# Optimization experiments

Hardware: AMD Instinct MI355X
Metric: run time of the kernel (lower is better)

Reference implementation:

```python
import jax, jax.numpy as jnp
import numpy as np

C_V, C_F, C_D = 10, 64, 16
COSTS = jnp.array([10.0, 5.0, 2.0], dtype=jnp.float32)  # bandwidth cost per granularity
PENALTY = 0.0  # no_transmission_utility_penalty


def setup_inputs() -> dict:
    key = jax.random.key(0)
    k1, k2 = jax.random.split(key)
    B, H, W = 4, 192, 192
    collab = jax.random.normal(k1, (B, C_V + C_F + C_D, H, W), dtype=jnp.float32)
    utility = jax.random.normal(k2, (B, H, W, 3), dtype=jnp.float32)
    return {"collab_bev_data_list": collab, "utility_map_list": utility,
            "bandwidth_budget": 200000}


def _selection_mechanism(utility, budget_per_sample):
    # utility: [B, H, W, G]; returns [B, H, W] float selected granularity (-1 = none)
    B, H, W, G = utility.shape
    best_u = jnp.max(utility, axis=3)                      # [B,H,W]
    best_g = jnp.argmax(utility, axis=3)                   # [B,H,W]
    N = B * H * W
    flat_u = best_u.reshape(N)
    flat_g = best_g.reshape(N)
    b_idx = jnp.repeat(jnp.arange(B, dtype=jnp.int32), H * W)
    valid = flat_u > PENALTY
    cost = COSTS[flat_g]                                   # [N]
    # sort candidates by utility, descending (stable, matching list.sort)
    order = jnp.argsort(-flat_u)
    v_s = valid[order]
    c_s = cost[order]
    b_s = b_idx[order]

    # greedy budget-constrained selection per sample (sequential knapsack)
    def step(usage, item):
        v, c, b = item
        ok = v & (usage[b] + c <= budget_per_sample)
        usage = usage.at[b].add(jnp.where(ok, c, jnp.float32(0)))
        return usage, ok

    _, sel_sorted = jax.lax.scan(step, jnp.zeros((B,), jnp.float32), (v_s, c_s, b_s))
    selected = jnp.zeros((N,), bool).at[order].set(sel_sorted)
    idx = jnp.where(selected, flat_g.astype(jnp.float32), jnp.float32(-1.0))
    return idx.reshape(B, H, W)


def _build_sparse_bev(sel_idx, vox, feat, det):
    m0 = (sel_idx == 0.0)[:, None, :, :]
    m1 = (sel_idx == 1.0)[:, None, :, :]
    m2 = (sel_idx == 2.0)[:, None, :, :]
    return jnp.concatenate([vox * m0, feat * m1, det * m2], axis=1)


def reference(collab_bev_data_list, utility_map_list, bandwidth_budget):
    cav_num = collab_bev_data_list.shape[0]
    budget_per_sample = jnp.float32(bandwidth_budget / cav_num)
    sel_idx = _selection_mechanism(utility_map_list, budget_per_sample)
    vox = collab_bev_data_list[:, :C_V]
    feat = collab_bev_data_list[:, C_V:C_V + C_F]
    det = collab_bev_data_list[:, C_V + C_F:C_V + C_F + C_D]
    sparse = _build_sparse_bev(sel_idx, vox, feat, det)
    return sparse, sel_idx
```

## Files before the change

### kernel.cpp

```cpp
#include <hip/hip_runtime.h>
#include <stdint.h>
#include <math.h>

#define B_    4
#define H_    192
#define W_    192
#define HW    (H_*W_)
#define NPIX  (B_*HW)
#define C_V   10
#define C_F   64
#define C_D   16
#define C_ALL (C_V+C_F+C_D)
#define HBINS 32768
#define CAP   2048

#define OFF_HIST 0u
#define OFF_KEY  (4u*HBINS*4u)
#define OFF_G    (OFF_KEY + (uint32_t)NPIX*4u)
#define OFF_SELX (OFF_G + (uint32_t)NPIX)
#define OFF_HL   (OFF_SELX + (uint32_t)NPIX)

__device__ __forceinline__ uint32_t costOf(uint32_t g) {
    return g == 0u ? 10u : (g == 1u ? 5u : 2u);
}

__device__ __forceinline__ uint32_t budgetInt(const int* bptr) {
    double bps = (double)bptr[0] / (double)B_;
    float f = (float)bps;
    return (uint32_t)floorf(f);
}

#define CE(x, y) { uint64_t _mn = (x) < (y) ? (x) : (y); \
                   uint64_t _mx = (x) < (y) ? (y) : (x); (x) = _mx; (y) = _mn; }

__global__ void k_zero(uint4* __restrict__ hist4) {
    int i = blockIdx.x * blockDim.x + threadIdx.x;
    hist4[i] = make_uint4(0u, 0u, 0u, 0u);
}

__global__ void k_prep(const float* __restrict__ util, uint4* __restrict__ key4,
                       uint32_t* __restrict__ g4, uint32_t* __restrict__ selx4,
                       uint32_t* __restrict__ hist) {
    int t = blockIdx.x * blockDim.x + threadIdx.x;
    if (t >= NPIX / 4) return;
    const float4* u4 = (const float4*)util + (size_t)t * 3;
    float4 a = u4[0], b4 = u4[1], c4 = u4[2];
    float u[4][3] = { {a.x, a.y, a.z}, {a.w, b4.x, b4.y},
                      {b4.z, b4.w, c4.x}, {c4.y, c4.z, c4.w} };
    uint32_t kk[4]; uint32_t gpack = 0;
    #pragma unroll
    for (int p = 0; p < 4; ++p) {
        float best = u[p][0]; uint32_t g = 0;
        if (u[p][1] > best) { best = u[p][1]; g = 1; }
        if (u[p][2] > best) { best = u[p][2]; g = 2; }
        kk[p] = (best > 0.0f) ? (__float_as_uint(best) | 0x80000000u) : 0u;
        gpack |= g << (8 * p);
    }
    key4[t] = make_uint4(kk[0], kk[1], kk[2], kk[3]);
    g4[t] = gpack;
    selx4[t] = 0u;
    int b = (t * 4) / HW;
    #pragma unroll
    for (int p = 0; p < 4; ++p)
        if (kk[p])
            atomicAdd(&hist[(size_t)b * HBINS + ((kk[p] >> 16) & 32767u)],
                      costOf((gpack >> (8 * p)) & 3u));
}

__global__ __launch_bounds__(1024) void k_select(const uint32_t* __restrict__ key,
                                                 const uint8_t* __restrict__ g,
                                                 const uint32_t* __restrict__ hist,
                                                 const int* __restrict__ budget_ptr,
                                                 uint8_t* __restrict__ selx,
                                                 uint32_t* __restrict__ hl_out) {
    int b = blockIdx.x;
    int t = threadIdx.x;
    int lane = t & 63, wv = t >> 6;
    uint32_t budget = budgetInt(budget_ptr);

    __shared__ uint64_t e[CAP];
    __shared__ uint64_t s[CAP];
    __shared__ uint32_t wsum[16];
    __shared__ uint64_t red5[16];
    __shared__ uint64_t red2[16][4];
    __shared__ uint64_t cand[5];
    __shared__ uint32_t f_b2, f_usage, sh_n, sh_r;

    if (t == 0) { f_b2 = 0xFFFFFFFFu; f_usage = 0u; sh_n = 0u; }
    __syncthreads();

    const uint32_t* hb = hist + (size_t)b * HBINS;
    int hi = 32767 - 32 * t;
    uint32_t cs = 0;
    #pragma unroll 4
    for (int j = 0; j < 32; ++j) cs += hb[hi - j];
    uint32_t v = cs;
    #pragma unroll
    for (int off = 1; off < 64; off <<= 1) {
        uint32_t o = __shfl_up(v, off);
        if (lane >= off) v += o;
    }
    if (lane == 63) wsum[wv] = v;
    __syncthreads();
    if (t < 16) {
        uint32_t w = wsum[t];
        #pragma unroll
        for (int off = 1; off < 16; off <<= 1) {
            uint32_t o = __shfl_up(w, off);
            if (t >= off) w += o;
        }
        wsum[t] = w;
    }
    __syncthreads();
    uint32_t incl = v + (wv ? wsum[wv - 1] : 0u);
    uint32_t excl = incl - cs;
    if (excl <= budget && incl > budget) {
        uint32_t cum = excl;
        for (int j = 0; j < 32; ++j) {
            uint32_t hv = hb[hi - j];
            if (cum + hv > budget) { f_b2 = (uint32_t)(hi - j); f_usage = cum; break; }
            cum += hv;
        }
    }
    __syncthreads();
    uint32_t b2 = f_b2;
    if (t == 0) {
        uint32_t hl;
        if (b2 == 0xFFFFFFFFu)           hl = 1u;
        else {
            uint32_t bs = b2 + 32768u;
            hl = (bs >= 65535u) ? 0xFFFFFFFFu : ((bs + 1u) << 16);
        }
        hl_out[b] = hl;
    }
    if (b2 == 0xFFFFFFFFu) return;

    const uint32_t* kb = key + (size_t)b * HW;
    const uint8_t*  gb = g   + (size_t)b * HW;
    uint64_t m5 = 0;
    uint64_t a0 = 0, a1 = 0, a2 = 0, a3 = 0;
    for (int i = t; i < HW; i += 1024) {
        uint32_t k = kb[i];
        if (!k) continue;
        uint32_t bin = (k >> 16) & 32767u;
        if (bin == b2) {
            uint32_t idx = atomicAdd(&sh_n, 1u);
            if (idx < CAP)
                e[idx] = ((uint64_t)(~k) << 32) | ((uint64_t)i << 2) | (uint64_t)gb[i];
        } else if (bin < b2) {
            uint32_t gg = gb[i];
            if (gg == 0u) continue;
            uint64_t m = ((uint64_t)k << 18) | ((uint64_t)(65535u - (uint32_t)i) << 2)
                       | (uint64_t)gg;
            if (gg == 1u) { if (m > m5) m5 = m; }
            else {
                if (m > a3) {
                    if      (m > a0) { a3 = a2; a2 = a1; a1 = a0; a0 = m; }
                    else if (m > a1) { a3 = a2; a2 = a1; a1 = m; }
                    else if (m > a2) { a3 = a2; a2 = m; }
                    else             { a3 = m; }
                }
            }
        }
    }
    #pragma unroll
    for (int off = 32; off; off >>= 1) {
        uint64_t o5 = __shfl_down(m5, off);
        if (o5 > m5) m5 = o5;
        uint64_t b0 = __shfl_down(a0, off), b1 = __shfl_down(a1, off),
                 b2_ = __shfl_down(a2, off), b3 = __shfl_down(a3, off);
        CE(a0, b3); CE(a1, b2_); CE(a2, b1); CE(a3, b0);
        CE(a0, a2); CE(a1, a3); CE(a0, a1); CE(a2, a3);
    }
    if (lane == 0) {
        red5[wv] = m5;
        red2[wv][0] = a0; red2[wv][1] = a1; red2[wv][2] = a2; red2[wv][3] = a3;
    }
    __syncthreads();
    int n = (int)(sh_n < (uint32_t)CAP ? sh_n : (uint32_t)CAP);

    for (int i = t; i < n; i += 1024) {
        uint64_t ei = e[i];
        int rk = 0;
        for (int j = 0; j < n; ++j) rk += (e[j] < ei);
        s[rk] = ei;
    }
    __syncthreads();

    if (t == 0) {
        uint32_t usage = f_usage;
        uint8_t* sx = selx + (size_t)b * HW;
        for (int i = 0; i < n; ++i) {
            uint64_t ei = s[i];
            uint32_t c = costOf((uint32_t)(ei & 3u));
            if (usage + c <= budget) { usage += c; sx[(ei >> 2) & 0xFFFFu] = 1; }
        }
        uint64_t g5 = 0, t0 = 0, t1 = 0, t2 = 0, t3 = 0;
        for (int wq = 0; wq < 16; ++wq) {
            if (red5[wq] > g5) g5 = red5[wq];
            #pragma unroll
            for (int q = 0; q < 4; ++q) {
                uint64_t m = red2[wq][q];
                if (m > t3) {
                    if      (m > t0) { t3 = t2; t2 = t1; t1 = t0; t0 = m; }
                    else if (m > t1) { t3 = t2; t2 = t1; t1 = m; }
                    else if (m > t2) { t3 = t2; t2 = m; }
                    else             { t3 = m; }
                }
            }
        }
        cand[0] = g5; cand[1] = t0; cand[2] = t1; cand[3] = t2; cand[4] = t3;
        for (int i = 1; i < 5; ++i) {
            uint64_t x = cand[i]; int j = i;
            while (j > 0 && cand[j - 1] < x) { cand[j] = cand[j - 1]; --j; }
            cand[j] = x;
        }
        uint32_t r = budget - usage;
        for (int i = 0; i < 5; ++i) {
            uint64_t m = cand[i];
            if (!m) break;
            uint32_t c = costOf((uint32_t)(m & 3u));
            if (c <= r) {
                r -= c;
                uint32_t pix = 65535u - (uint32_t)((m >> 2) & 0xFFFFu);
                sx[pix] = 1;
            }
        }
        sh_r = r; (void)sh_r;
    }
}

__global__ void k_sparse(const float* __restrict__ collab, const uint4* __restrict__ key4,
                         const uint32_t* __restrict__ g4, const uint32_t* __restrict__ selx4,
                         const uint32_t* __restrict__ hl_arr,
                         float* __restrict__ out, float* __restrict__ selOut) {
    int tid = blockIdx.x * blockDim.x + threadIdx.x;
    int c = blockIdx.y, b = blockIdx.z;
    int cls = (c < C_V) ? 0 : ((c < C_V + C_F) ? 1 : 2);
    uint32_t hl = hl_arr[b];
    size_t p4 = (size_t)b * (HW / 4) + (size_t)tid;
    uint4 kk = key4[p4];
    uint32_t gg = g4[p4];
    uint32_t sx = selx4[p4];
    int sc[4];
    uint32_t kv[4] = { kk.x, kk.y, kk.z, kk.w };
    #pragma unroll
    for (int p = 0; p < 4; ++p) {
        bool se = (kv[p] >= hl) || (((sx >> (8 * p)) & 0xFFu) != 0u);
        sc[p] = se ? (int)((gg >> (8 * p)) & 3u) : -1;
    }
    size_t co = ((size_t)(b * C_ALL + c)) * HW + (size_t)tid * 4;
    float4 v = *(const float4*)(collab + co);
    float4 o;
    o.x = (sc[0] == cls) ? v.x : 0.0f;
    o.y = (sc[1] == cls) ? v.y : 0.0f;
    o.z = (sc[2] == cls) ? v.z : 0.0f;
    o.w = (sc[3] == cls) ? v.w : 0.0f;
    *(float4*)(out + co) = o;
    if (c == 0) {
        float4 sf = make_float4((float)sc[0], (float)sc[1], (float)sc[2], (float)sc[3]);
        ((float4*)selOut)[p4] = sf;
    }
}

extern "C" void kernel_launch(void* const* d_in, const int* in_sizes, int n_in,
                              void* d_out, int out_size, void* d_ws, size_t ws_size,
                              hipStream_t stream) {
    (void)in_sizes; (void)n_in; (void)out_size; (void)ws_size;
    const float* collab = (const float*)d_in[0];
    const float* util   = (const float*)d_in[1];
    const int*   budget = (const int*)d_in[2];

    uint8_t*  ws   = (uint8_t*)d_ws;
    uint32_t* hist = (uint32_t*)(ws + OFF_HIST);
    uint32_t* key  = (uint32_t*)(ws + OFF_KEY);
    uint8_t*  g    = ws + OFF_G;
    uint8_t*  selx = ws + OFF_SELX;
    uint32_t* hl   = (uint32_t*)(ws + OFF_HL);

    float* outSparse = (float*)d_out;
    float* outSel    = outSparse + (size_t)B_ * C_ALL * HW;

    k_zero  <<<(4 * HBINS / 4) / 256, 256, 0, stream>>>((uint4*)hist);
    k_prep  <<<(NPIX / 4 + 255) / 256, 256, 0, stream>>>(util, (uint4*)key,
                                                         (uint32_t*)g, (uint32_t*)selx, hist);
    k_select<<<B_, 1024, 0, stream>>>(key, g, hist, budget, selx, hl);
    dim3 grid3(HW / 4 / 256, C_ALL, B_);
    k_sparse<<<grid3, 256, 0, stream>>>(collab, (const uint4*)key, (const uint32_t*)g,
                                        (const uint32_t*)selx, hl, outSparse, outSel);
}
```

Before: 107.5 us.

## Split per-sample selection kernel into coarse cut, parallel gather and final pass

Replaces the single 4-block selection kernel with three stages. A two-level histogram (a 256-bin coarse histogram plus the fine one) locates the budget cutoff bin with one wave per sample. A gather kernel spread over 36 slices per sample collects boundary-bin items and top candidates through global atomics and lists. A small final kernel ranks the boundary items and applies the greedy fill. This is meant to remove the serial scan over the whole image done by only four blocks, at the cost of two extra launches, extra coarse-histogram atomics and global-memory round trips.

```diff
diff --git a/kernel.cpp b/kernel.cpp
--- a/kernel.cpp
+++ b/kernel.cpp
@@ -12,13 +12,21 @@
 #define C_D   16
 #define C_ALL (C_V+C_F+C_D)
 #define HBINS 32768
+#define CBINS 256
 #define CAP   2048
-
-#define OFF_HIST 0u
-#define OFF_KEY  (4u*HBINS*4u)
-#define OFF_G    (OFF_KEY + (uint32_t)NPIX*4u)
-#define OFF_SELX (OFF_G + (uint32_t)NPIX)
-#define OFF_HL   (OFF_SELX + (uint32_t)NPIX)
+#define NSLICE 36
+#define NCAND (NSLICE*5)
+
+#define OFF_HIST   0u
+#define OFF_COARSE (4u*HBINS*4u)
+#define ZERO_U4    ((OFF_COARSE + 4u*CBINS*4u)/16u)
+#define OFF_KEY    (OFF_COARSE + 4u*CBINS*4u)
+#define OFF_G      (OFF_KEY + (uint32_t)NPIX*4u)
+#define OFF_SELX   (OFF_G + (uint32_t)NPIX)
+#define OFF_RES    (OFF_SELX + (uint32_t)NPIX)
+#define OFF_GCNT   (OFF_RES + 48u)
+#define OFF_GLIST  (OFF_GCNT + 16u)
+#define OFF_CAND   (OFF_GLIST + 4u*CAP*8u)
 
 __device__ __forceinline__ uint32_t costOf(uint32_t g) {
     return g == 0u ? 10u : (g == 1u ? 5u : 2u);
@@ -33,14 +41,14 @@
 #define CE(x, y) { uint64_t _mn = (x) < (y) ? (x) : (y); \
                    uint64_t _mx = (x) < (y) ? (y) : (x); (x) = _mx; (y) = _mn; }
 
-__global__ void k_zero(uint4* __restrict__ hist4) {
-    int i = blockIdx.x * blockDim.x + threadIdx.x;
-    hist4[i] = make_uint4(0u, 0u, 0u, 0u);
+__global__ void k_zero(uint4* __restrict__ w4) {
+    uint32_t i = blockIdx.x * blockDim.x + threadIdx.x;
+    if (i < ZERO_U4) w4[i] = make_uint4(0u, 0u, 0u, 0u);
 }
 
 __global__ void k_prep(const float* __restrict__ util, uint4* __restrict__ key4,
                        uint32_t* __restrict__ g4, uint32_t* __restrict__ selx4,
-                       uint32_t* __restrict__ hist) {
+                       uint32_t* __restrict__ hist, uint32_t* __restrict__ coarse) {
     int t = blockIdx.x * blockDim.x + threadIdx.x;
     if (t >= NPIX / 4) return;
     const float4* u4 = (const float4*)util + (size_t)t * 3;
@@ -62,104 +70,114 @@
     int b = (t * 4) / HW;
     #pragma unroll
     for (int p = 0; p < 4; ++p)
-        if (kk[p])
-            atomicAdd(&hist[(size_t)b * HBINS + ((kk[p] >> 16) & 32767u)],
-                      costOf((gpack >> (8 * p)) & 3u));
-}
-
-__global__ __launch_bounds__(1024) void k_select(const uint32_t* __restrict__ key,
-                                                 const uint8_t* __restrict__ g,
-                                                 const uint32_t* __restrict__ hist,
-                                                 const int* __restrict__ budget_ptr,
-                                                 uint8_t* __restrict__ selx,
-                                                 uint32_t* __restrict__ hl_out) {
-    int b = blockIdx.x;
+        if (kk[p]) {
+            uint32_t c = costOf((gpack >> (8 * p)) & 3u);
+            atomicAdd(&hist[(size_t)b * HBINS + ((kk[p] >> 16) & 32767u)], c);
+            atomicAdd(&coarse[(size_t)b * CBINS + ((kk[p] >> 23) & 0xFFu)], c);
+        }
+}
+
+__global__ __launch_bounds__(256) void k_cut(const uint32_t* __restrict__ coarse,
+                                             const uint32_t* __restrict__ hist,
+                                             const int* __restrict__ budget_ptr,
+                                             uint32_t* __restrict__ res,
+                                             uint32_t* __restrict__ gcnt) {
     int t = threadIdx.x;
-    int lane = t & 63, wv = t >> 6;
+    int b = t >> 6, lane = t & 63;
     uint32_t budget = budgetInt(budget_ptr);
 
-    __shared__ uint64_t e[CAP];
-    __shared__ uint64_t s[CAP];
-    __shared__ uint32_t wsum[16];
-    __shared__ uint64_t red5[16];
-    __shared__ uint64_t red2[16][4];
-    __shared__ uint64_t cand[5];
-    __shared__ uint32_t f_b2, f_usage, sh_n, sh_r;
-
-    if (t == 0) { f_b2 = 0xFFFFFFFFu; f_usage = 0u; sh_n = 0u; }
-    __syncthreads();
-
-    const uint32_t* hb = hist + (size_t)b * HBINS;
-    int hi = 32767 - 32 * t;
-    uint32_t cs = 0;
-    #pragma unroll 4
-    for (int j = 0; j < 32; ++j) cs += hb[hi - j];
+    const uint32_t* cb_ = coarse + (size_t)b * CBINS;
+    int hi = 255 - 4 * lane;
+    uint32_t c0 = cb_[hi], c1 = cb_[hi - 1], c2 = cb_[hi - 2], c3 = cb_[hi - 3];
+    uint32_t cs = c0 + c1 + c2 + c3;
     uint32_t v = cs;
     #pragma unroll
     for (int off = 1; off < 64; off <<= 1) {
         uint32_t o = __shfl_up(v, off);
         if (lane >= off) v += o;
     }
-    if (lane == 63) wsum[wv] = v;
-    __syncthreads();
-    if (t < 16) {
-        uint32_t w = wsum[t];
-        #pragma unroll
-        for (int off = 1; off < 16; off <<= 1) {
-            uint32_t o = __shfl_up(w, off);
-            if (t >= off) w += o;
-        }
-        wsum[t] = w;
-    }
-    __syncthreads();
-    uint32_t incl = v + (wv ? wsum[wv - 1] : 0u);
-    uint32_t excl = incl - cs;
-    if (excl <= budget && incl > budget) {
+    uint32_t excl = v - cs;
+    bool found = (excl <= budget) && (v > budget);
+    uint32_t cbin = 0, cusage = 0;
+    if (found) {
         uint32_t cum = excl;
-        for (int j = 0; j < 32; ++j) {
-            uint32_t hv = hb[hi - j];
-            if (cum + hv > budget) { f_b2 = (uint32_t)(hi - j); f_usage = cum; break; }
-            cum += hv;
-        }
-    }
-    __syncthreads();
-    uint32_t b2 = f_b2;
-    if (t == 0) {
-        uint32_t hl;
-        if (b2 == 0xFFFFFFFFu)           hl = 1u;
-        else {
-            uint32_t bs = b2 + 32768u;
-            hl = (bs >= 65535u) ? 0xFFFFFFFFu : ((bs + 1u) << 16);
-        }
-        hl_out[b] = hl;
-    }
+        if      (cum + c0 > budget) { cbin = (uint32_t)hi;     cusage = cum; }
+        else if ((cum += c0) + c1 > budget) { cbin = (uint32_t)(hi - 1); cusage = cum; }
+        else if ((cum += c1) + c2 > budget) { cbin = (uint32_t)(hi - 2); cusage = cum; }
+        else                        { cbin = (uint32_t)(hi - 3); cusage = cum + c2; }
+    }
+    unsigned long long msk = __ballot(found);
+    if (msk == 0ull) {
+        if (lane == 0) { res[b] = 0xFFFFFFFFu; res[4 + b] = 0u; res[8 + b] = 1u;
+                         gcnt[b] = 0u; }
+        return;
+    }
+    int src = __ffsll((long long)msk) - 1;
+    cbin   = __shfl(cbin, src);
+    cusage = __shfl(cusage, src);
+
+    const uint32_t* hb = hist + (size_t)b * HBINS + (size_t)cbin * 128;
+    int fhi = 127 - 2 * lane;
+    uint32_t f0 = hb[fhi], f1 = hb[fhi - 1];
+    uint32_t fs = f0 + f1;
+    v = fs;
+    #pragma unroll
+    for (int off = 1; off < 64; off <<= 1) {
+        uint32_t o = __shfl_up(v, off);
+        if (lane >= off) v += o;
+    }
+    excl = cusage + v - fs;
+    found = (excl <= budget) && (excl + fs > budget);
+    uint32_t b2 = 0, fusage = 0;
+    if (found) {
+        if (excl + f0 > budget) { b2 = cbin * 128u + (uint32_t)fhi;       fusage = excl; }
+        else                    { b2 = cbin * 128u + (uint32_t)(fhi - 1); fusage = excl + f0; }
+    }
+    msk = __ballot(found);
+    src = __ffsll((long long)msk) - 1;
+    b2     = __shfl(b2, src);
+    fusage = __shfl(fusage, src);
+    if (lane == 0) {
+        res[b]     = b2;
+        res[4 + b] = fusage;
+        uint32_t bs = b2 + 32768u;
+        res[8 + b] = (bs >= 65535u) ? 0xFFFFFFFFu : ((bs + 1u) << 16);
+        gcnt[b] = 0u;
+    }
+}
+
+__global__ __launch_bounds__(1024) void k_gather(const uint32_t* __restrict__ key,
+                                                 const uint8_t* __restrict__ g,
+                                                 const uint32_t* __restrict__ res,
+                                                 uint32_t* __restrict__ gcnt,
+                                                 uint64_t* __restrict__ glist,
+                                                 uint64_t* __restrict__ cand) {
+    int b = blockIdx.y;
+    uint32_t b2 = res[b];
     if (b2 == 0xFFFFFFFFu) return;
-
-    const uint32_t* kb = key + (size_t)b * HW;
-    const uint8_t*  gb = g   + (size_t)b * HW;
-    uint64_t m5 = 0;
-    uint64_t a0 = 0, a1 = 0, a2 = 0, a3 = 0;
-    for (int i = t; i < HW; i += 1024) {
-        uint32_t k = kb[i];
-        if (!k) continue;
+    int t = threadIdx.x;
+    int lane = t & 63, wv = t >> 6;
+    uint32_t pix = blockIdx.x * 1024u + (uint32_t)t;
+
+    __shared__ uint64_t red5[16];
+    __shared__ uint64_t red2[16][4];
+
+    uint32_t k = key[(size_t)b * HW + pix];
+    uint64_t m5 = 0, a0 = 0, a1 = 0, a2 = 0, a3 = 0;
+    if (k) {
         uint32_t bin = (k >> 16) & 32767u;
         if (bin == b2) {
-            uint32_t idx = atomicAdd(&sh_n, 1u);
+            uint32_t gg = g[(size_t)b * HW + pix];
+            uint32_t idx = atomicAdd(&gcnt[b], 1u);
             if (idx < CAP)
-                e[idx] = ((uint64_t)(~k) << 32) | ((uint64_t)i << 2) | (uint64_t)gb[i];
+                glist[(size_t)b * CAP + idx] =
+                    ((uint64_t)(~k) << 32) | ((uint64_t)pix << 2) | (uint64_t)gg;
         } else if (bin < b2) {
-            uint32_t gg = gb[i];
-            if (gg == 0u) continue;
-            uint64_t m = ((uint64_t)k << 18) | ((uint64_t)(65535u - (uint32_t)i) << 2)
-                       | (uint64_t)gg;
-            if (gg == 1u) { if (m > m5) m5 = m; }
-            else {
-                if (m > a3) {
-                    if      (m > a0) { a3 = a2; a2 = a1; a1 = a0; a0 = m; }
-                    else if (m > a1) { a3 = a2; a2 = a1; a1 = m; }
-                    else if (m > a2) { a3 = a2; a2 = m; }
-                    else             { a3 = m; }
-                }
+            uint32_t gg = g[(size_t)b * HW + pix];
+            if (gg) {
+                uint64_t m = ((uint64_t)k << 18) | ((uint64_t)(65535u - pix) << 2)
+                           | (uint64_t)gg;
+                if (gg == 1u) m5 = m; else a0 = m;
             }
         }
     }
@@ -177,24 +195,7 @@
         red2[wv][0] = a0; red2[wv][1] = a1; red2[wv][2] = a2; red2[wv][3] = a3;
     }
     __syncthreads();
-    int n = (int)(sh_n < (uint32_t)CAP ? sh_n : (uint32_t)CAP);
-
-    for (int i = t; i < n; i += 1024) {
-        uint64_t ei = e[i];
-        int rk = 0;
-        for (int j = 0; j < n; ++j) rk += (e[j] < ei);
-        s[rk] = ei;
-    }
-    __syncthreads();
-
     if (t == 0) {
-        uint32_t usage = f_usage;
-        uint8_t* sx = selx + (size_t)b * HW;
-        for (int i = 0; i < n; ++i) {
-            uint64_t ei = s[i];
-            uint32_t c = costOf((uint32_t)(ei & 3u));
-            if (usage + c <= budget) { usage += c; sx[(ei >> 2) & 0xFFFFu] = 1; }
-        }
         uint64_t g5 = 0, t0 = 0, t1 = 0, t2 = 0, t3 = 0;
         for (int wq = 0; wq < 16; ++wq) {
             if (red5[wq] > g5) g5 = red5[wq];
@@ -209,15 +210,70 @@
                 }
             }
         }
-        cand[0] = g5; cand[1] = t0; cand[2] = t1; cand[3] = t2; cand[4] = t3;
+        uint64_t* cb_ = cand + ((size_t)b * NSLICE + blockIdx.x) * 5;
+        cb_[0] = g5; cb_[1] = t0; cb_[2] = t1; cb_[3] = t2; cb_[4] = t3;
+    }
+}
+
+__global__ __launch_bounds__(256) void k_final(const uint32_t* __restrict__ res,
+                                               const uint32_t* __restrict__ gcnt,
+                                               const uint64_t* __restrict__ glist,
+                                               const uint64_t* __restrict__ cand,
+                                               const int* __restrict__ budget_ptr,
+                                               uint8_t* __restrict__ selx) {
+    int b = blockIdx.x;
+    uint32_t b2 = res[b];
+    if (b2 == 0xFFFFFFFFu) return;
+    int t = threadIdx.x;
+
+    __shared__ uint64_t e[CAP];
+    __shared__ uint64_t s[CAP];
+    __shared__ uint64_t cd[NCAND];
+
+    uint32_t cnt = gcnt[b];
+    int n = (int)(cnt < (uint32_t)CAP ? cnt : (uint32_t)CAP);
+    for (int i = t; i < n; i += 256) e[i] = glist[(size_t)b * CAP + i];
+    for (int i = t; i < NCAND; i += 256) cd[i] = cand[(size_t)b * NCAND + i];
+    __syncthreads();
+
+    for (int i = t; i < n; i += 256) {
+        uint64_t ei = e[i];
+        int rk = 0;
+        for (int j = 0; j < n; ++j) rk += (e[j] < ei);
+        s[rk] = ei;
+    }
+    __syncthreads();
+
+    if (t == 0) {
+        uint32_t budget = budgetInt(budget_ptr);
+        uint32_t usage = res[4 + b];
+        uint8_t* sx = selx + (size_t)b * HW;
+        for (int i = 0; i < n; ++i) {
+            uint64_t ei = s[i];
+            uint32_t c = costOf((uint32_t)(ei & 3u));
+            if (usage + c <= budget) { usage += c; sx[(ei >> 2) & 0xFFFFu] = 1; }
+        }
+        uint64_t g5 = 0, t0 = 0, t1 = 0, t2 = 0, t3 = 0;
+        for (int i = 0; i < NCAND; ++i) {
+            uint64_t m = cd[i];
+            if (!m) continue;
+            if ((m & 3u) == 1u) { if (m > g5) g5 = m; }
+            else if (m > t3) {
+                if      (m > t0) { t3 = t2; t2 = t1; t1 = t0; t0 = m; }
+                else if (m > t1) { t3 = t2; t2 = t1; t1 = m; }
+                else if (m > t2) { t3 = t2; t2 = m; }
+                else             { t3 = m; }
+            }
+        }
+        uint64_t c5[5] = { g5, t0, t1, t2, t3 };
         for (int i = 1; i < 5; ++i) {
-            uint64_t x = cand[i]; int j = i;
-            while (j > 0 && cand[j - 1] < x) { cand[j] = cand[j - 1]; --j; }
-            cand[j] = x;
+            uint64_t x = c5[i]; int j = i;
+            while (j > 0 && c5[j - 1] < x) { c5[j] = c5[j - 1]; --j; }
+            c5[j] = x;
         }
         uint32_t r = budget - usage;
         for (int i = 0; i < 5; ++i) {
-            uint64_t m = cand[i];
+            uint64_t m = c5[i];
             if (!m) break;
             uint32_t c = costOf((uint32_t)(m & 3u));
             if (c <= r) {
@@ -226,7 +282,6 @@
                 sx[pix] = 1;
             }
         }
-        sh_r = r; (void)sh_r;
     }
 }
 
@@ -271,21 +326,28 @@
     const float* util   = (const float*)d_in[1];
     const int*   budget = (const int*)d_in[2];
 
-    uint8_t*  ws   = (uint8_t*)d_ws;
-    uint32_t* hist = (uint32_t*)(ws + OFF_HIST);
-    uint32_t* key  = (uint32_t*)(ws + OFF_KEY);
-    uint8_t*  g    = ws + OFF_G;
-    uint8_t*  selx = ws + OFF_SELX;
-    uint32_t* hl   = (uint32_t*)(ws + OFF_HL);
+    uint8_t*  ws     = (uint8_t*)d_ws;
+    uint32_t* hist   = (uint32_t*)(ws + OFF_HIST);
+    uint32_t* coarse = (uint32_t*)(ws + OFF_COARSE);
+    uint32_t* key    = (uint32_t*)(ws + OFF_KEY);
+    uint8_t*  g      = ws + OFF_G;
+    uint8_t*  selx   = ws + OFF_SELX;
+    uint32_t* res    = (uint32_t*)(ws + OFF_RES);
+    uint32_t* gcnt   = (uint32_t*)(ws + OFF_GCNT);
+    uint64_t* glist  = (uint64_t*)(ws + OFF_GLIST);
+    uint64_t* cand   = (uint64_t*)(ws + OFF_CAND);
 
     float* outSparse = (float*)d_out;
     float* outSel    = outSparse + (size_t)B_ * C_ALL * HW;
 
-    k_zero  <<<(4 * HBINS / 4) / 256, 256, 0, stream>>>((uint4*)hist);
-    k_prep  <<<(NPIX / 4 + 255) / 256, 256, 0, stream>>>(util, (uint4*)key,
-                                                         (uint32_t*)g, (uint32_t*)selx, hist);
-    k_select<<<B_, 1024, 0, stream>>>(key, g, hist, budget, selx, hl);
+    k_zero  <<<(ZERO_U4 + 255) / 256, 256, 0, stream>>>((uint4*)ws);
+    k_prep  <<<(NPIX / 4 + 255) / 256, 256, 0, stream>>>(util, (uint4*)key, (uint32_t*)g,
+                                                         (uint32_t*)selx, hist, coarse);
+    k_cut   <<<1, 256, 0, stream>>>(coarse, hist, budget, res, gcnt);
+    dim3 gridG(NSLICE, B_);
+    k_gather<<<gridG, 1024, 0, stream>>>(key, g, res, gcnt, glist, cand);
+    k_final <<<B_, 256, 0, stream>>>(res, gcnt, glist, cand, budget, selx);
     dim3 grid3(HW / 4 / 256, C_ALL, B_);
     k_sparse<<<grid3, 256, 0, stream>>>(collab, (const uint4*)key, (const uint32_t*)g,
-                                        (const uint32_t*)selx, hl, outSparse, outSel);
-}
+                                        (const uint32_t*)selx, res + 8, outSparse, outSel);
+}
```

Measured after the change: 257.2 us. 2.39x slower.
